# Performance work log

Hardware: AMD Instinct MI355X
Metric: run time of the kernel (lower is better)

## Reference

```python
import jax, jax.numpy as jnp
import numpy as np

BASE_CHUNK = 64
MAX_SEQ_LEN = 256
HIDDEN = 128
DIST_CORE = 6.0
DIST_SHELL = 10.0


def _linear_params(key, fan_in, fan_out):
    lim = 1.0 / np.sqrt(fan_in)
    kw, kb = jax.random.split(key)
    W = jax.random.uniform(kw, (fan_in, fan_out), jnp.float32, -lim, lim)
    b = jax.random.uniform(kb, (fan_out,), jnp.float32, -lim, lim)
    return W, b


def setup_inputs() -> dict:
    key = jax.random.key(0)
    ks = jax.random.split(key, 8)
    B, S, De = 16, 768, 16
    node_features = jax.random.normal(ks[0], (B, S, HIDDEN), jnp.float32)
    # channel 0 acts as a pairwise distance; uniform in [0, 20) spans core/shell thresholds
    edge_features = jax.random.uniform(ks[1], (B, S, S, De), jnp.float32) * 20.0
    sequence_mask = jnp.ones((B, S), jnp.float32)
    pocket_mask = jax.random.bernoulli(ks[2], 0.02, (B, S))
    W_node, b_node = _linear_params(ks[3], HIDDEN, 32)
    W_e1, b_e1 = _linear_params(ks[4], 1, 64)
    W_e2, b_e2 = _linear_params(ks[5], 64, 32)
    W_imp, b_imp = _linear_params(ks[6], 64, 1)
    return dict(node_features=node_features, edge_features=edge_features,
                sequence_mask=sequence_mask, pocket_mask=pocket_mask,
                W_node=W_node, b_node=b_node, W_e1=W_e1, b_e1=b_e1,
                W_e2=W_e2, b_e2=b_e2, W_imp=W_imp, b_imp=b_imp)


def reference(node_features, edge_features, sequence_mask, pocket_mask,
              W_node, b_node, W_e1, b_e1, W_e2, b_e2, W_imp, b_imp):
    B, S, _ = node_features.shape
    adj = min(BASE_CHUNK, MAX_SEQ_LEN // 4) if S > MAX_SEQ_LEN else BASE_CHUNK  # static

    node_enc = node_features @ W_node + b_node                      # [B,S,32]
    edge_summary = edge_features.mean(axis=-1).mean(axis=-1)[..., None]  # [B,S,1]
    h = jax.nn.relu(edge_summary @ W_e1 + b_e1)                     # [B,S,64]
    edge_enc = h @ W_e2 + b_e2                                      # [B,S,32]
    combined = jnp.concatenate([node_enc, edge_enc], axis=-1)       # [B,S,64]
    importance = jax.nn.sigmoid(combined @ W_imp + b_imp) * sequence_mask[..., None]  # [B,S,1]
    imp = importance[..., 0]                                        # [B,S]

    # ---- pocket branch (vectorized over batch) ----
    # min distance from each node to any pocket node (inf where no pocket)
    dist = jnp.where(pocket_mask[:, None, :], edge_features[..., 0], jnp.inf).min(axis=2)  # [B,S]
    core = dist < DIST_CORE
    imp_mean = imp.mean(axis=1, keepdims=True)
    shell = (dist >= DIST_CORE) & (dist < DIST_SHELL) & (imp > imp_mean)
    merged = pocket_mask | core | shell
    merged_len = jnp.minimum(merged.sum(axis=1), MAX_SEQ_LEN)       # clamp (argsort path keeps max_seq_len)
    chunk_pocket = jnp.minimum(jnp.maximum(merged_len, adj), MAX_SEQ_LEN).astype(jnp.float32)

    # ---- no-pocket branch ----
    imp_full = importance.mean(axis=(1, 2))                          # [B]
    chunk_np = jnp.clip(BASE_CHUNK * imp_full,
                        float(adj // 2), float(min(adj * 2, MAX_SEQ_LEN)))

    has_pocket = pocket_mask.any(axis=1)
    chunk_sizes = jnp.where(has_pocket, chunk_pocket, chunk_np)      # [B]
    return chunk_sizes, MAX_SEQ_LEN
```

## Files before the change

### kernel.cpp

```cpp
#include <hip/hip_runtime.h>
#include <hip/hip_bf16.h>
#include <math.h>

#define BB 16
#define SS 768
#define DE 16
#define HID 128


__global__ __launch_bounds__(256) void setup_kernel(
    const unsigned int* __restrict__ pm,
    const float* __restrict__ Wn, const float* __restrict__ bn,
    const float* __restrict__ We2, const float* __restrict__ be2,
    const float* __restrict__ Wimp, const float* __restrict__ bimp,
    float* __restrict__ ws) {
    const int tid = threadIdx.x;
    if (blockIdx.x == 0) {
        __shared__ int bad;
        if (tid == 0) bad = 0;
        __syncthreads();
        for (int t = tid; t < (BB * SS) / 4; t += 256) {
            unsigned int w = pm[t];
            if (w > 1u && w != 0x3F800000u) bad = 1;
        }
        __syncthreads();
        if (tid == 0) ((int*)ws)[0] = bad;
    } else {
        if (tid < 128) {
            float s = 0.f;
            for (int c = 0; c < 32; ++c) s += Wn[tid * 32 + c] * Wimp[c];
            ws[16 + tid] = s;
        }
        if (tid < 64) {
            float s = 0.f;
            for (int c = 0; c < 32; ++c) s += We2[tid * 32 + c] * Wimp[32 + c];
            ws[144 + tid] = s;
        }
        if (tid == 0) {
            float s = bimp[0];
            for (int c = 0; c < 32; ++c) s += bn[c] * Wimp[c];
            for (int c = 0; c < 32; ++c) s += be2[c] * Wimp[32 + c];
            ws[208] = s;
        }
    }
}

__global__ __launch_bounds__(256) void edge_kernel(
    const float4* __restrict__ edge, const float* __restrict__ nf,
    const void* __restrict__ pmask, const float* __restrict__ seqmask,
    const float* __restrict__ We1, const float* __restrict__ be1,
    float* __restrict__ ws) {
    const int tid = threadIdx.x;
    const int lane = tid & 63;
    const int wid = tid >> 6;
    const int bi = blockIdx.x * 4 + wid;
    const int b = blockIdx.x / (SS / 4);

    __shared__ unsigned char s_m[SS];
    const int flag = ((const int*)ws)[0];
    if (flag) {
        const unsigned char* pm = (const unsigned char*)pmask + (size_t)b * SS;
        for (int j = tid; j < SS; j += 256) s_m[j] = pm[j] ? 1 : 0;
    } else {
        const unsigned int* pm = (const unsigned int*)pmask + (size_t)b * SS;
        for (int j = tid; j < SS; j += 256) s_m[j] = pm[j] ? 1 : 0;
    }
    __syncthreads();

    const float nf0 = nf[(size_t)bi * HID + lane];
    const float nf1 = nf[(size_t)bi * HID + 64 + lane];

    const float4* row = edge + (size_t)bi * (SS * DE / 4);
    float sum = 0.f;
    float dmin = INFINITY;
    const bool ch0 = (lane & 3) == 0;
    const int j0 = lane >> 2;
#pragma unroll 8
    for (int k = 0; k < 48; ++k) {
        float4 v = row[lane + (k << 6)];
        sum += (v.x + v.y) + (v.z + v.w);
        if (ch0) {
            if (s_m[j0 + (k << 4)]) dmin = fminf(dmin, v.x);
        }
    }

#pragma unroll
    for (int m = 32; m > 0; m >>= 1) {
        sum += __shfl_xor(sum, m, 64);
        dmin = fminf(dmin, __shfl_xor(dmin, m, 64));
    }

    const float es = sum * (1.0f / (float)(SS * DE));
    float p = nf0 * ws[16 + lane] + nf1 * ws[16 + 64 + lane];
    float h = fmaxf(es * We1[lane] + be1[lane], 0.f);
    p += h * ws[144 + lane];
#pragma unroll
    for (int m = 32; m > 0; m >>= 1) p += __shfl_xor(p, m, 64);

    if (lane == 0) {
        float logit = p + ws[208];
        float impv = seqmask[bi] / (1.f + expf(-logit));
        ws[256 + bi] = impv;
        ws[256 + BB * SS + bi] = dmin;
    }
}

__global__ __launch_bounds__(256) void final_kernel(
    const void* __restrict__ pmask, const float* __restrict__ ws,
    float* __restrict__ out) {
    const int tid = threadIdx.x;
    const int b = blockIdx.x;
    __shared__ float s_f[256];
    __shared__ int s_i[256];

    const float* imp = ws + 256;
    const float* dist = ws + 256 + BB * SS;
    const int flag = ((const int*)ws)[0];

    float psum = 0.f;
    int por = 0;
    for (int i = tid; i < SS; i += 256) {
        psum += imp[b * SS + i];
        int m = flag ? (((const unsigned char*)pmask)[b * SS + i] != 0)
                     : (((const unsigned int*)pmask)[b * SS + i] != 0u);
        por |= m;
    }
    s_f[tid] = psum;
    s_i[tid] = por;
    __syncthreads();
    for (int off = 128; off > 0; off >>= 1) {
        if (tid < off) {
            s_f[tid] += s_f[tid + off];
            s_i[tid] |= s_i[tid + off];
        }
        __syncthreads();
    }
    const float imp_mean = s_f[0] / (float)SS;
    const int haspocket = s_i[0];
    __syncthreads();

    int cnt = 0;
    for (int i = tid; i < SS; i += 256) {
        int m = flag ? (((const unsigned char*)pmask)[b * SS + i] != 0)
                     : (((const unsigned int*)pmask)[b * SS + i] != 0u);
        float d = dist[b * SS + i];
        bool core = d < 6.0f;
        bool shell = (d >= 6.0f) && (d < 10.0f) && (imp[b * SS + i] > imp_mean);
        cnt += (m || core || shell) ? 1 : 0;
    }
    s_i[tid] = cnt;
    __syncthreads();
    for (int off = 128; off > 0; off >>= 1) {
        if (tid < off) s_i[tid] += s_i[tid + off];
        __syncthreads();
    }
    if (tid == 0) {
        float chunk;
        if (haspocket) {
            float ml = fminf((float)s_i[0], 256.f);
            chunk = fminf(fmaxf(ml, 64.f), 256.f);
        } else {
            chunk = fminf(fmaxf(64.f * imp_mean, 32.f), 128.f);
        }
        out[b] = chunk;
        if (b == 0) out[BB] = 256.f;
    }
}

extern "C" void kernel_launch(void* const* d_in, const int* in_sizes, int n_in,
                              void* d_out, int out_size, void* d_ws, size_t ws_size,
                              hipStream_t stream) {
    const float* nf = (const float*)d_in[0];
    const float4* edge = (const float4*)d_in[1];
    const float* seqmask = (const float*)d_in[2];
    const void* pmask = d_in[3];
    const float* Wn = (const float*)d_in[4];
    const float* bn = (const float*)d_in[5];
    const float* We1 = (const float*)d_in[6];
    const float* be1 = (const float*)d_in[7];
    const float* We2 = (const float*)d_in[8];
    const float* be2 = (const float*)d_in[9];
    const float* Wimp = (const float*)d_in[10];
    const float* bimp = (const float*)d_in[11];
    float* ws = (float*)d_ws;
    float* out = (float*)d_out;

    setup_kernel<<<2, 256, 0, stream>>>((const unsigned int*)pmask,
                                        Wn, bn, We2, be2, Wimp, bimp, ws);
    edge_kernel<<<(BB * SS) / 4, 256, 0, stream>>>(edge, nf, pmask, seqmask, We1, be1, ws);
    final_kernel<<<BB, 256, 0, stream>>>(pmask, ws, out);
}
```

Measured before the change: 798.3 us.

## Split edge reduction into grid-stride chunk pass and per-row finalize kernel

The row-per-wave edge reduction becomes two kernels. The first is a persistent grid-stride kernel in which each wave reduces one 1 KB chunk (sum and masked min), reading the pocket mask from global memory, and writes partials to workspace. The second kernel combines the 48 partials per row and computes importance. This aims to raise memory-level parallelism on the 600 MB edge stream. It adds a full wave reduction per chunk, more workspace traffic and an extra launch.

```diff
diff --git a/kernel.cpp b/kernel.cpp
--- a/kernel.cpp
+++ b/kernel.cpp
@@ -1,12 +1,18 @@
 #include <hip/hip_runtime.h>
-#include <hip/hip_bf16.h>
 #include <math.h>
 
 #define BB 16
 #define SS 768
 #define DE 16
 #define HID 128
-
+#define NROW (BB * SS)
+#define CPR 48
+#define NCHUNK (NROW * CPR)
+
+#define WS_IMP 256
+#define WS_DST (256 + NROW)
+#define WS_SUM 32768
+#define WS_MIN (32768 + NCHUNK)
 
 __global__ __launch_bounds__(256) void setup_kernel(
     const unsigned int* __restrict__ pm,
@@ -45,63 +51,67 @@
     }
 }
 
-__global__ __launch_bounds__(256) void edge_kernel(
-    const float4* __restrict__ edge, const float* __restrict__ nf,
-    const void* __restrict__ pmask, const float* __restrict__ seqmask,
+__global__ __launch_bounds__(256) void edgeA_kernel(
+    const float4* __restrict__ edge, const void* __restrict__ pmask,
+    float* __restrict__ ws) {
+    const int lane = threadIdx.x & 63;
+    const int gw = (blockIdx.x * 256 + threadIdx.x) >> 6;
+    const int nw = (gridDim.x * 256) >> 6;
+    const int flag = ((const int*)ws)[0];
+    const bool ch0 = (lane & 3) == 0;
+
+    for (int c = gw; c < NCHUNK; c += nw) {
+        const float4 v = edge[((size_t)c << 6) + lane];
+        float s = (v.x + v.y) + (v.z + v.w);
+        float dm = INFINITY;
+        if (ch0) {
+            const int row = c / CPR;
+            const int cc = c - row * CPR;
+            const int b = row / SS;
+            const int j = (cc << 4) + (lane >> 2);
+            int m = flag ? (((const unsigned char*)pmask)[b * SS + j] != 0)
+                         : (((const unsigned int*)pmask)[(size_t)b * SS + j] != 0u);
+            if (m) dm = v.x;
+        }
+#pragma unroll
+        for (int x = 32; x > 0; x >>= 1) {
+            s += __shfl_xor(s, x, 64);
+            dm = fminf(dm, __shfl_xor(dm, x, 64));
+        }
+        if (lane == 0) {
+            ws[WS_SUM + c] = s;
+            ws[WS_MIN + c] = dm;
+        }
+    }
+}
+
+__global__ __launch_bounds__(256) void edgeB_kernel(
+    const float* __restrict__ nf, const float* __restrict__ seqmask,
     const float* __restrict__ We1, const float* __restrict__ be1,
     float* __restrict__ ws) {
-    const int tid = threadIdx.x;
-    const int lane = tid & 63;
-    const int wid = tid >> 6;
-    const int bi = blockIdx.x * 4 + wid;
-    const int b = blockIdx.x / (SS / 4);
-
-    __shared__ unsigned char s_m[SS];
-    const int flag = ((const int*)ws)[0];
-    if (flag) {
-        const unsigned char* pm = (const unsigned char*)pmask + (size_t)b * SS;
-        for (int j = tid; j < SS; j += 256) s_m[j] = pm[j] ? 1 : 0;
-    } else {
-        const unsigned int* pm = (const unsigned int*)pmask + (size_t)b * SS;
-        for (int j = tid; j < SS; j += 256) s_m[j] = pm[j] ? 1 : 0;
-    }
-    __syncthreads();
-
-    const float nf0 = nf[(size_t)bi * HID + lane];
-    const float nf1 = nf[(size_t)bi * HID + 64 + lane];
-
-    const float4* row = edge + (size_t)bi * (SS * DE / 4);
-    float sum = 0.f;
-    float dmin = INFINITY;
-    const bool ch0 = (lane & 3) == 0;
-    const int j0 = lane >> 2;
-#pragma unroll 8
-    for (int k = 0; k < 48; ++k) {
-        float4 v = row[lane + (k << 6)];
-        sum += (v.x + v.y) + (v.z + v.w);
-        if (ch0) {
-            if (s_m[j0 + (k << 4)]) dmin = fminf(dmin, v.x);
-        }
-    }
-
+    const int lane = threadIdx.x & 63;
+    const int bi = blockIdx.x * 4 + (threadIdx.x >> 6);
+
+    float s = (lane < CPR) ? ws[WS_SUM + bi * CPR + lane] : 0.f;
+    float dm = (lane < CPR) ? ws[WS_MIN + bi * CPR + lane] : INFINITY;
 #pragma unroll
-    for (int m = 32; m > 0; m >>= 1) {
-        sum += __shfl_xor(sum, m, 64);
-        dmin = fminf(dmin, __shfl_xor(dmin, m, 64));
-    }
-
-    const float es = sum * (1.0f / (float)(SS * DE));
-    float p = nf0 * ws[16 + lane] + nf1 * ws[16 + 64 + lane];
+    for (int x = 32; x > 0; x >>= 1) {
+        s += __shfl_xor(s, x, 64);
+        dm = fminf(dm, __shfl_xor(dm, x, 64));
+    }
+
+    const float es = s * (1.0f / (float)(SS * DE));
+    float p = nf[(size_t)bi * HID + lane] * ws[16 + lane]
+            + nf[(size_t)bi * HID + 64 + lane] * ws[16 + 64 + lane];
     float h = fmaxf(es * We1[lane] + be1[lane], 0.f);
     p += h * ws[144 + lane];
 #pragma unroll
-    for (int m = 32; m > 0; m >>= 1) p += __shfl_xor(p, m, 64);
+    for (int x = 32; x > 0; x >>= 1) p += __shfl_xor(p, x, 64);
 
     if (lane == 0) {
         float logit = p + ws[208];
-        float impv = seqmask[bi] / (1.f + expf(-logit));
-        ws[256 + bi] = impv;
-        ws[256 + BB * SS + bi] = dmin;
+        ws[WS_IMP + bi] = seqmask[bi] / (1.f + expf(-logit));
+        ws[WS_DST + bi] = dm;
     }
 }
 
@@ -113,8 +123,8 @@
     __shared__ float s_f[256];
     __shared__ int s_i[256];
 
-    const float* imp = ws + 256;
-    const float* dist = ws + 256 + BB * SS;
+    const float* imp = ws + WS_IMP;
+    const float* dist = ws + WS_DST;
     const int flag = ((const int*)ws)[0];
 
     float psum = 0.f;
@@ -187,6 +197,7 @@
 
     setup_kernel<<<2, 256, 0, stream>>>((const unsigned int*)pmask,
                                         Wn, bn, We2, be2, Wimp, bimp, ws);
-    edge_kernel<<<(BB * SS) / 4, 256, 0, stream>>>(edge, nf, pmask, seqmask, We1, be1, ws);
+    edgeA_kernel<<<2048, 256, 0, stream>>>(edge, pmask, ws);
+    edgeB_kernel<<<NROW / 4, 256, 0, stream>>>(nf, seqmask, We1, be1, ws);
     final_kernel<<<BB, 256, 0, stream>>>(pmask, ws, out);
 }
```

After: 800.5 us. Within noise of the previous version (+0.3%).
